# Performance work log

Hardware: AMD Instinct MI355X
Metric: run time of the kernel (lower is better)

Reference implementation:

```python
import jax, jax.numpy as jnp
import numpy as np

DIM = 1024
H = 16
HEAD_DIM = 64
HIDDEN = H * HEAD_DIM  # == DIM, required by the module's reshape
SCALE = HEAD_DIM ** -0.5


def setup_inputs() -> dict:
    key = jax.random.key(0)
    k_x, k_qkv, k_w1, k_b1 = jax.random.split(key, 4)
    B, N = 8, 1024
    x = jax.random.normal(k_x, (B, N, DIM), dtype=jnp.float32)
    # nn.Linear stores weight as [out, in]; we keep [in, out] for x @ W
    w_qkv = jax.random.normal(k_qkv, (DIM, 3 * HIDDEN), dtype=jnp.float32) * (DIM ** -0.5)
    w_out = jax.random.normal(k_w1, (HIDDEN, DIM), dtype=jnp.float32) * (HIDDEN ** -0.5)
    b_out = jax.random.normal(k_b1, (DIM,), dtype=jnp.float32) * 0.02
    return {"x": x, "w_qkv": w_qkv, "w_out": w_out, "b_out": b_out}


def reference(x, w_qkv, w_out, b_out):
    B, N, C = x.shape
    # QKV projection (no bias), split into heads
    qkv = (x @ w_qkv).reshape(B, N, 3, H, C // H)
    q, k, v = qkv[:, :, 0], qkv[:, :, 1], qkv[:, :, 2]  # [B, N, H, d]
    attn = jnp.einsum("bqhd,bkhd->bhqk", q, k) * SCALE
    attn = jax.nn.softmax(attn, axis=-1)  # dropout inactive at eval
    out = jnp.einsum("bhqk,bkhd->bqhd", attn, v).reshape(B, N, C)
    return out @ w_out + b_out
```

## Files before the change

### kernel.cpp

```cpp
#include <hip/hip_runtime.h>
#include <hip/hip_bf16.h>

#define B_SZ 8
#define SEQ 1024
#define DIM_ 1024
#define NH 16
#define HD 64
#define M_TOT (B_SZ*SEQ)
#define N_QKV (3*DIM_)

typedef __attribute__((ext_vector_type(8))) short bf16x8;
typedef __attribute__((ext_vector_type(4))) float f32x4;

typedef const __attribute__((address_space(1))) void gvoid;
typedef __attribute__((address_space(3))) void lvoid;

__device__ __forceinline__ short f2bf(float f){
  union { __hip_bfloat16 h; short s; } u;
  u.h = __float2bfloat16(f);
  return u.s;
}

__global__ void cvt_kernel(const float* __restrict__ in, short* __restrict__ out, int n4){
  int i = blockIdx.x*blockDim.x + threadIdx.x;
  int stride = gridDim.x*blockDim.x;
  for (; i < n4; i += stride){
    float4 v = reinterpret_cast<const float4*>(in)[i];
    short4 s;
    s.x = f2bf(v.x); s.y = f2bf(v.y); s.z = f2bf(v.z); s.w = f2bf(v.w);
    reinterpret_cast<short4*>(out)[i] = s;
  }
}

__global__ void tconv_kernel(const float* __restrict__ in, short* __restrict__ out, int R, int C){
  __shared__ alignas(16) short tile[64][66];
  const int l = threadIdx.x & 63, w = threadIdx.x >> 6;
  const int r0 = blockIdx.y * 64, c0 = blockIdx.x * 64;
  #pragma unroll
  for (int rr = 0; rr < 16; ++rr){
    int r = w + rr*4;
    tile[r][l] = f2bf(in[(size_t)(r0+r)*C + c0 + l]);
  }
  __syncthreads();
  #pragma unroll
  for (int cc = 0; cc < 16; ++cc){
    int c = w + cc*4;
    out[(size_t)(c0+c)*R + r0 + l] = tile[l][c];
  }
}

template<int EPI, int GX, int NOFF>
__global__ __launch_bounds__(256, 4) void gemm5(
    const short* __restrict__ A, const short* __restrict__ Bt,
    int M, int Nn, int K,
    short* __restrict__ Qb, short* __restrict__ Kb, short* __restrict__ Vtb,
    const float* __restrict__ bias, float* __restrict__ outF)
{
  __shared__ alignas(16) short As[2][128*32];
  __shared__ alignas(16) short Bs[2][128*32];

  const int orig = blockIdx.x;
  const int xcd = orig & 7, t = orig >> 3;
  const int by = xcd*8 + t/GX, bx = t % GX;

  const int tid = threadIdx.x;
  const int l = tid & 63, wid = tid >> 6;
  const int wr = wid >> 1, wc = wid & 1;
  const int lr = l & 15, lw = l >> 4;
  const int sw = (lr >> 1) & 3;
  const int m0 = by * 128, n0 = (bx + NOFF) * 128;

  f32x4 acc[4][4];
  const f32x4 zz = {0.f,0.f,0.f,0.f};
  #pragma unroll
  for (int m=0;m<4;m++)
    #pragma unroll
    for (int n=0;n<4;n++) acc[m][n] = zz;

  auto STAGE = [&](int buf, int kt){
    const int k0 = kt << 5;
    #pragma unroll
    for (int j=0;j<2;j++){
      const int idx = j*256 + tid;
      const int row = idx >> 2;
      const int ws  = (idx & 3) ^ ((row >> 1) & 3);
      __builtin_amdgcn_global_load_lds(
          (gvoid*)(A + (size_t)(m0+row)*K + k0 + ws*8),
          (lvoid*)(&As[buf][idx*8]), 16, 0, 0);
    }
    #pragma unroll
    for (int j=0;j<2;j++){
      const int idx = j*256 + tid;
      const int row = idx >> 2;
      const int ws  = (idx & 3) ^ ((row >> 1) & 3);
      __builtin_amdgcn_global_load_lds(
          (gvoid*)(Bt + (size_t)(n0+row)*K + k0 + ws*8),
          (lvoid*)(&Bs[buf][idx*8]), 16, 0, 0);
    }
  };

  STAGE(0, 0);
  __syncthreads();

  const int NT = K >> 5;
  int buf = 0;
  for (int kt = 0; kt < NT; ++kt){
    if (kt + 1 < NT) STAGE(buf ^ 1, kt + 1);

    bf16x8 af[4], bfr[4];
    const int wsel = (lw ^ sw) << 3;
    #pragma unroll
    for (int m=0;m<4;m++){
      const int r = wr*64 + m*16 + lr;
      af[m] = *(const bf16x8*)(&As[buf][r*32 + wsel]);
    }
    #pragma unroll
    for (int n=0;n<4;n++){
      const int r = wc*64 + n*16 + lr;
      bfr[n] = *(const bf16x8*)(&Bs[buf][r*32 + wsel]);
    }
    #pragma unroll
    for (int m=0;m<4;m++)
      #pragma unroll
      for (int n=0;n<4;n++)
        acc[m][n] = __builtin_amdgcn_mfma_f32_16x16x32_bf16(af[m], bfr[n], acc[m][n], 0, 0, 0);

    __syncthreads();
    buf ^= 1;
  }

  #pragma unroll
  for (int n=0;n<4;n++){
    const int col = n0 + wc*64 + n*16 + lr;
    if (EPI == 0){
      const int three = col >> 10;
      const int cc = col & 1023;
      const int h = cc >> 6, d = cc & 63;
      #pragma unroll
      for (int m=0;m<4;m++){
        const int rbase = m0 + wr*64 + m*16 + (lw<<2);
        const int b = rbase >> 10, nn = rbase & 1023;
        const int bh = b*NH + h;
        if (three == 2){
          short4 pk;
          pk.x = f2bf(acc[m][n][0]); pk.y = f2bf(acc[m][n][1]);
          pk.z = f2bf(acc[m][n][2]); pk.w = f2bf(acc[m][n][3]);
          *(short4*)(&Vtb[((size_t)bh*HD + d)*SEQ + nn]) = pk;
        } else if (three == 0){
          #pragma unroll
          for (int ri=0;ri<4;ri++)
            Qb[((size_t)bh*SEQ + nn + ri)*HD + d] = f2bf(acc[m][n][ri] * 0.1803368801f);
        } else {
          #pragma unroll
          for (int ri=0;ri<4;ri++)
            Kb[((size_t)bh*SEQ + nn + ri)*HD + d] = f2bf(acc[m][n][ri]);
        }
      }
    } else {
      const float bv = bias[col];
      #pragma unroll
      for (int m=0;m<4;m++){
        const int rbase = m0 + wr*64 + m*16 + (lw<<2);
        #pragma unroll
        for (int ri=0;ri<4;ri++)
          outF[(size_t)(rbase+ri)*Nn + col] = acc[m][n][ri] + bv;
      }
    }
  }
}

__global__ __launch_bounds__(256) void attn_kernel(
    const short* __restrict__ Q, const short* __restrict__ Kb,
    const short* __restrict__ Vt, short* __restrict__ Ao)
{
  __shared__ alignas(16) short Ks[2][64*64];
  __shared__ alignas(16) short Vs[2][64*64];
  __shared__ alignas(16) short Ps[4][16*72];

  const int tid = threadIdx.x;
  const int l = tid & 63, w = tid >> 6;
  const int bid = blockIdx.x;
  const int qt = bid & 15, bh = bid >> 4;
  const int b = bh >> 4, h = bh & 15;
  const size_t base = (size_t)bh << 16;

  const int lr = l & 15;
  const int q4 = l >> 4;
  const int lk = q4 << 3;
  const int sw8 = lr & 7;

  const int qrow = qt*64 + w*16 + lr;
  const short* qp = Q + base + (size_t)qrow*HD + lk;
  const bf16x8 qf0 = *(const bf16x8*)qp;
  const bf16x8 qf1 = *(const bf16x8*)(qp + 32);

  float m_run = -1e30f, l_run = 0.f;
  f32x4 o[4];
  #pragma unroll
  for (int i=0;i<4;i++) o[i] = f32x4{0.f,0.f,0.f,0.f};

  bf16x8 kr[2], vr[2];
  auto load_tile = [&](int kt){
    const int kv0 = kt*64;
    #pragma unroll
    for (int p=0;p<2;p++){
      const int idx = tid + p*256;
      const int row = idx >> 3, c8 = (idx & 7) << 3;
      kr[p] = *(const bf16x8*)(Kb + base + (size_t)(kv0+row)*HD + c8);
      vr[p] = *(const bf16x8*)(Vt + base + (size_t)row*SEQ + kv0 + c8);
    }
  };
  auto write_tile = [&](int bi){
    #pragma unroll
    for (int p=0;p<2;p++){
      const int idx = tid + p*256;
      const int row = idx >> 3;
      const int wsw = ((idx & 7) ^ (row & 7)) << 3;
      *(bf16x8*)(&Ks[bi][row*64 + wsw]) = kr[p];
      *(bf16x8*)(&Vs[bi][row*64 + wsw]) = vr[p];
    }
  };

  load_tile(0);
  write_tile(0);
  __syncthreads();

  int cur = 0;
  for (int kt = 0; kt < 16; ++kt){
    if (kt < 15) load_tile(kt+1);

    const short* kb = &Ks[cur][0];
    const short* vb = &Vs[cur][0];

    f32x4 s[4];
    #pragma unroll
    for (int cg=0;cg<4;cg++) s[cg] = f32x4{0.f,0.f,0.f,0.f};
    __builtin_amdgcn_s_setprio(1);
    #pragma unroll
    for (int cg=0;cg<4;cg++){
      const short* kp = kb + (cg*16 + lr)*64;
      bf16x8 kf0 = *(const bf16x8*)(kp + ((q4     ^ sw8) << 3));
      bf16x8 kf1 = *(const bf16x8*)(kp + (((q4+4) ^ sw8) << 3));
      s[cg] = __builtin_amdgcn_mfma_f32_16x16x32_bf16(kf0, qf0, s[cg], 0,0,0);
      s[cg] = __builtin_amdgcn_mfma_f32_16x16x32_bf16(kf1, qf1, s[cg], 0,0,0);
    }
    __builtin_amdgcn_s_setprio(0);

    float m0_ = fmaxf(fmaxf(s[0][0], s[0][1]), fmaxf(s[0][2], s[0][3]));
    float m1_ = fmaxf(fmaxf(s[1][0], s[1][1]), fmaxf(s[1][2], s[1][3]));
    float m2_ = fmaxf(fmaxf(s[2][0], s[2][1]), fmaxf(s[2][2], s[2][3]));
    float m3_ = fmaxf(fmaxf(s[3][0], s[3][1]), fmaxf(s[3][2], s[3][3]));
    float mt = fmaxf(fmaxf(m0_, m1_), fmaxf(m2_, m3_));
    mt = fmaxf(mt, __shfl_xor(mt, 16));
    mt = fmaxf(mt, __shfl_xor(mt, 32));

    if (!__all(mt - m_run <= 8.0f)){
      const float mn = fmaxf(m_run, mt);
      const float corr = __builtin_amdgcn_exp2f(m_run - mn);
      m_run = mn;
      l_run *= corr;
      float corr_r[4];
      #pragma unroll
      for (int ri=0;ri<4;ri++) corr_r[ri] = __shfl(corr, (q4<<2) + ri);
      #pragma unroll
      for (int dg=0;dg<4;dg++)
        #pragma unroll
        for (int ri=0;ri<4;ri++) o[dg][ri] *= corr_r[ri];
    }

    float rs = 0.f;
    short* pw = &Ps[w][0];
    #pragma unroll
    for (int cg=0;cg<4;cg++){
      float p0 = __builtin_amdgcn_exp2f(s[cg][0] - m_run);
      float p1 = __builtin_amdgcn_exp2f(s[cg][1] - m_run);
      float p2 = __builtin_amdgcn_exp2f(s[cg][2] - m_run);
      float p3 = __builtin_amdgcn_exp2f(s[cg][3] - m_run);
      rs += (p0+p1)+(p2+p3);
      short4 pk; pk.x=f2bf(p0); pk.y=f2bf(p1); pk.z=f2bf(p2); pk.w=f2bf(p3);
      *(short4*)(pw + lr*72 + cg*16 + q4*4) = pk;
    }
    rs += __shfl_xor(rs, 16);
    rs += __shfl_xor(rs, 32);
    l_run += rs;

    const bf16x8 pa0 = *(const bf16x8*)(pw + lr*72 + lk);
    const bf16x8 pa1 = *(const bf16x8*)(pw + lr*72 + lk + 32);
    __builtin_amdgcn_s_setprio(1);
    #pragma unroll
    for (int dg=0;dg<4;dg++){
      const short* vp = vb + (dg*16 + lr)*64;
      bf16x8 vf0 = *(const bf16x8*)(vp + ((q4     ^ sw8) << 3));
      bf16x8 vf1 = *(const bf16x8*)(vp + (((q4+4) ^ sw8) << 3));
      o[dg] = __builtin_amdgcn_mfma_f32_16x16x32_bf16(pa0, vf0, o[dg], 0,0,0);
      o[dg] = __builtin_amdgcn_mfma_f32_16x16x32_bf16(pa1, vf1, o[dg], 0,0,0);
    }
    __builtin_amdgcn_s_setprio(0);

    if (kt < 15) write_tile(cur ^ 1);
    __syncthreads();
    cur ^= 1;
  }

  float linv[4];
  #pragma unroll
  for (int ri=0;ri<4;ri++) linv[ri] = 1.0f / __shfl(l_run, (q4<<2) + ri);
  #pragma unroll
  for (int ri=0;ri<4;ri++){
    const int row = qt*64 + w*16 + (q4<<2) + ri;
    short* op = Ao + ((size_t)(b*SEQ + row))*DIM_ + h*HD;
    #pragma unroll
    for (int dg=0;dg<4;dg++)
      op[dg*16 + lr] = f2bf(o[dg][ri] * linv[ri]);
  }
}

extern "C" void kernel_launch(void* const* d_in, const int* in_sizes, int n_in,
                              void* d_out, int out_size, void* d_ws, size_t ws_size,
                              hipStream_t stream)
{
  (void)in_sizes; (void)n_in; (void)out_size; (void)ws_size;
  const float* x     = (const float*)d_in[0];
  const float* w_qkv = (const float*)d_in[1];
  const float* w_out = (const float*)d_in[2];
  const float* b_out = (const float*)d_in[3];
  float* out = (float*)d_out;

  char* ws = (char*)d_ws;
  const size_t MB = (size_t)1 << 20;
  short* xb    = (short*)(ws);
  short* wqkvT = (short*)(ws + 16*MB);
  short* woutT = (short*)(ws + 22*MB);
  short* Qb    = (short*)(ws + 24*MB);
  short* Kb    = (short*)(ws + 40*MB);
  short* Vtb   = (short*)(ws + 56*MB);
  short* Aob   = (short*)(ws + 72*MB);

  cvt_kernel<<<2048, 256, 0, stream>>>(x, xb, (M_TOT*DIM_)/4);
  tconv_kernel<<<dim3(N_QKV/64, DIM_/64), 256, 0, stream>>>(w_qkv, wqkvT, DIM_, N_QKV);
  tconv_kernel<<<dim3(DIM_/64, DIM_/64), 256, 0, stream>>>(w_out, woutT, DIM_, DIM_);

  gemm5<0,16,0><<<1024, 256, 0, stream>>>(
      xb, wqkvT, M_TOT, N_QKV, DIM_, Qb, Kb, Vtb, nullptr, nullptr);

  gemm5<0,8,16><<<512, 256, 0, stream>>>(
      xb, wqkvT, M_TOT, N_QKV, DIM_, Qb, Kb, Vtb, nullptr, nullptr);

  attn_kernel<<<B_SZ*NH*(SEQ/64), 256, 0, stream>>>(Qb, Kb, Vtb, Aob);

  gemm5<1,8,0><<<512, 256, 0, stream>>>(
      Aob, woutT, M_TOT, DIM_, DIM_, nullptr, nullptr, nullptr, b_out, out);
}
```

Baseline: 185.3 us.

## Load K/V attention fragments directly from global memory, dropping LDS staging

Removes the double-buffered shared-memory staging of K and V tiles in the attention kernel. Each wave now reads its MFMA operand fragments straight from global memory (relying on L1/L2 caching, since all 4 waves read the same K/V), which eliminates the LDS writes, swizzling and the per-iteration block barrier. The cost is 4x redundant global/cache traffic per block, with load latency exposed because nothing is prefetched ahead of use.

```diff
diff --git a/kernel.cpp b/kernel.cpp
--- a/kernel.cpp
+++ b/kernel.cpp
@@ -173,8 +173,6 @@
     const short* __restrict__ Q, const short* __restrict__ Kb,
     const short* __restrict__ Vt, short* __restrict__ Ao)
 {
-  __shared__ alignas(16) short Ks[2][64*64];
-  __shared__ alignas(16) short Vs[2][64*64];
   __shared__ alignas(16) short Ps[4][16*72];
 
   const int tid = threadIdx.x;
@@ -187,50 +185,22 @@
   const int lr = l & 15;
   const int q4 = l >> 4;
   const int lk = q4 << 3;
-  const int sw8 = lr & 7;
 
   const int qrow = qt*64 + w*16 + lr;
   const short* qp = Q + base + (size_t)qrow*HD + lk;
   const bf16x8 qf0 = *(const bf16x8*)qp;
   const bf16x8 qf1 = *(const bf16x8*)(qp + 32);
 
+  const short* kfp = Kb + base + (size_t)lr*HD + lk;
+  const short* vfp = Vt + base + (size_t)lr*SEQ + lk;
+
   float m_run = -1e30f, l_run = 0.f;
   f32x4 o[4];
   #pragma unroll
   for (int i=0;i<4;i++) o[i] = f32x4{0.f,0.f,0.f,0.f};
 
-  bf16x8 kr[2], vr[2];
-  auto load_tile = [&](int kt){
-    const int kv0 = kt*64;
-    #pragma unroll
-    for (int p=0;p<2;p++){
-      const int idx = tid + p*256;
-      const int row = idx >> 3, c8 = (idx & 7) << 3;
-      kr[p] = *(const bf16x8*)(Kb + base + (size_t)(kv0+row)*HD + c8);
-      vr[p] = *(const bf16x8*)(Vt + base + (size_t)row*SEQ + kv0 + c8);
-    }
-  };
-  auto write_tile = [&](int bi){
-    #pragma unroll
-    for (int p=0;p<2;p++){
-      const int idx = tid + p*256;
-      const int row = idx >> 3;
-      const int wsw = ((idx & 7) ^ (row & 7)) << 3;
-      *(bf16x8*)(&Ks[bi][row*64 + wsw]) = kr[p];
-      *(bf16x8*)(&Vs[bi][row*64 + wsw]) = vr[p];
-    }
-  };
-
-  load_tile(0);
-  write_tile(0);
-  __syncthreads();
-
-  int cur = 0;
   for (int kt = 0; kt < 16; ++kt){
-    if (kt < 15) load_tile(kt+1);
-
-    const short* kb = &Ks[cur][0];
-    const short* vb = &Vs[cur][0];
+    const int kv0 = kt << 6;
 
     f32x4 s[4];
     #pragma unroll
@@ -238,9 +208,9 @@
     __builtin_amdgcn_s_setprio(1);
     #pragma unroll
     for (int cg=0;cg<4;cg++){
-      const short* kp = kb + (cg*16 + lr)*64;
-      bf16x8 kf0 = *(const bf16x8*)(kp + ((q4     ^ sw8) << 3));
-      bf16x8 kf1 = *(const bf16x8*)(kp + (((q4+4) ^ sw8) << 3));
+      const short* kp = kfp + (size_t)(kv0 + cg*16)*HD;
+      bf16x8 kf0 = *(const bf16x8*)kp;
+      bf16x8 kf1 = *(const bf16x8*)(kp + 32);
       s[cg] = __builtin_amdgcn_mfma_f32_16x16x32_bf16(kf0, qf0, s[cg], 0,0,0);
       s[cg] = __builtin_amdgcn_mfma_f32_16x16x32_bf16(kf1, qf1, s[cg], 0,0,0);
     }
@@ -289,17 +259,13 @@
     __builtin_amdgcn_s_setprio(1);
     #pragma unroll
     for (int dg=0;dg<4;dg++){
-      const short* vp = vb + (dg*16 + lr)*64;
-      bf16x8 vf0 = *(const bf16x8*)(vp + ((q4     ^ sw8) << 3));
-      bf16x8 vf1 = *(const bf16x8*)(vp + (((q4+4) ^ sw8) << 3));
+      const short* vp = vfp + (size_t)(dg*16)*SEQ + kv0;
+      bf16x8 vf0 = *(const bf16x8*)vp;
+      bf16x8 vf1 = *(const bf16x8*)(vp + 32);
       o[dg] = __builtin_amdgcn_mfma_f32_16x16x32_bf16(pa0, vf0, o[dg], 0,0,0);
       o[dg] = __builtin_amdgcn_mfma_f32_16x16x32_bf16(pa1, vf1, o[dg], 0,0,0);
     }
     __builtin_amdgcn_s_setprio(0);
-
-    if (kt < 15) write_tile(cur ^ 1);
-    __syncthreads();
-    cur ^= 1;
   }
 
   float linv[4];
```

Result: slower. 360.2 us (+94.4%).
